# Performance work log

Hardware: AMD Instinct MI355X
Metric: run time of the kernel (lower is better)

## Reference

```python
import jax, jax.numpy as jnp
import numpy as np

N_NODES = 20000
N_EDGES = 200000
F = 132            # features_dim
DEGREES = (1, 2, 3)
REPEATS = jnp.array([3, 5, 7])   # 2l+1
EV_DIM = 15
H_INV, D_INV = 4, 33   # num_heads, inv_head_dim
H_EV, D_EV = 3, 44     # len(degrees), ev_head_dim
NRB = 32


def so3_invariants(x, y):
    # per-degree inner product over the (2l+1) components -> [E, len(degrees)]
    p = x * y
    return jnp.stack([p[:, 0:3].sum(-1), p[:, 3:8].sum(-1), p[:, 8:15].sum(-1)], axis=-1)


def filter_net(rbf, evi, Wr1, br1, Wr2, br2, We1, be1, We2, be2):
    # mlp_rbf: Linear(nrb,F)->SiLU->Linear(F,F); mlp_ev: Linear(3,F//4)->SiLU->Linear(F//4,F)
    r = jax.nn.silu(rbf @ Wr1 + br1) @ Wr2 + br2
    e = jax.nn.silu(evi @ We1 + be1) @ We2 + be2
    return r + e


def setup_inputs() -> dict:
    key = jax.random.key(0)
    ks = jax.random.split(key, 32)
    s = 0.05
    inp = {
        'inv_features': jax.random.normal(ks[0], (N_NODES, F), jnp.float32),
        'ev_features': jax.random.normal(ks[1], (N_NODES, EV_DIM), jnp.float32),
        'rbf': jax.random.uniform(ks[2], (N_EDGES, NRB), jnp.float32),
        'senders': jax.random.randint(ks[3], (N_EDGES,), 0, N_NODES, jnp.int32),
        'receivers': jax.random.randint(ks[4], (N_EDGES,), 0, N_NODES, jnp.int32),
        'sh_vectors': jax.random.normal(ks[5], (N_EDGES, EV_DIM), jnp.float32),
        'cutoffs': jax.random.uniform(ks[6], (N_EDGES, 1), jnp.float32),
        # attention weights
        'W_q_inv': jax.random.normal(ks[7], (H_INV, D_INV, D_INV), jnp.float32) * s,
        'W_k_inv': jax.random.normal(ks[8], (H_INV, D_INV, D_INV), jnp.float32) * s,
        'W_v_inv': jax.random.normal(ks[9], (H_INV, D_INV, D_INV), jnp.float32) * s,
        'W_q_ev': jax.random.normal(ks[10], (H_EV, D_EV, D_EV), jnp.float32) * s,
        'W_k_ev': jax.random.normal(ks[11], (H_EV, D_EV, D_EV), jnp.float32) * s,
    }
    # two FilterNets (inv and ev), stored as [in,out] matrices
    for tag, base in (('fi', 12), ('fe', 20)):
        inp[f'{tag}_rbf_W1'] = jax.random.normal(ks[base + 0], (NRB, F), jnp.float32) * s
        inp[f'{tag}_rbf_b1'] = jnp.zeros((F,), jnp.float32)
        inp[f'{tag}_rbf_W2'] = jax.random.normal(ks[base + 1], (F, F), jnp.float32) * s
        inp[f'{tag}_rbf_b2'] = jnp.zeros((F,), jnp.float32)
        inp[f'{tag}_ev_W1'] = jax.random.normal(ks[base + 2], (len(DEGREES), F // 4), jnp.float32) * s
        inp[f'{tag}_ev_b1'] = jnp.zeros((F // 4,), jnp.float32)
        inp[f'{tag}_ev_W2'] = jax.random.normal(ks[base + 3], (F // 4, F), jnp.float32) * s
        inp[f'{tag}_ev_b2'] = jnp.zeros((F,), jnp.float32)
    # interaction block linear: (F+len(degrees)) -> (F+len(degrees))
    inp['W_int'] = jax.random.normal(ks[28], (F + len(DEGREES), F + len(DEGREES)), jnp.float32) * s
    inp['b_int'] = jnp.zeros((F + len(DEGREES),), jnp.float32)
    return inp


def _forward(inv_features, ev_features, rbf, sh_vectors, cutoffs,
             W_q_inv, W_k_inv, W_v_inv, W_q_ev, W_k_ev,
             fi, fe, W_int, b_int, senders, receivers):
    E = rbf.shape[0]
    N = inv_features.shape[0]
    # ---- EuclideanAttentionBlock ----
    ev_diff = ev_features[senders] - ev_features[receivers]          # [E, 15]
    evi = so3_invariants(ev_diff, ev_diff)                            # [E, 3]
    fw_inv = filter_net(rbf, evi, *fi).reshape(E, H_INV, D_INV)
    fw_ev = filter_net(rbf, evi, *fe).reshape(E, H_EV, D_EV)
    x_inv = inv_features.reshape(N, H_INV, D_INV)
    x_ev = inv_features.reshape(N, H_EV, D_EV)
    q_inv = jnp.einsum('Hij,NHi->NHj', W_q_inv, x_inv)[receivers]
    k_inv = jnp.einsum('Hij,NHi->NHj', W_k_inv, x_inv)[senders]
    v_inv = jnp.einsum('Hij,NHi->NHj', W_v_inv, x_inv)[senders]
    q_ev = jnp.einsum('Hij,NHi->NHj', W_q_ev, x_ev)[receivers]
    k_ev = jnp.einsum('Hij,NHi->NHj', W_k_ev, x_ev)[senders]
    alpha_inv = (q_inv * k_inv * fw_inv).sum(-1, keepdims=True) / np.sqrt(D_INV)  # [E,H,1]
    scaled_inv = cutoffs[:, None] * alpha_inv * v_inv                 # [E,H,D]
    d_inv = jax.ops.segment_sum(scaled_inv, receivers, num_segments=N).reshape(N, F)
    alpha_ev = (q_ev * k_ev * fw_ev).sum(-1) / np.sqrt(D_EV)          # [E,3]
    alpha_ev = jnp.repeat(alpha_ev, REPEATS, axis=-1, total_repeat_length=EV_DIM)
    d_ev = jax.ops.segment_sum(cutoffs * alpha_ev * sh_vectors, receivers, num_segments=N)
    att_inv = inv_features + d_inv
    att_ev = ev_features + d_ev
    # ---- InteractionBlock ----
    evi2 = so3_invariants(att_ev, att_ev)                             # [N,3]
    t = jnp.concatenate([att_inv, evi2], axis=-1) @ W_int + b_int
    d_inv2, b_ev = t[:, :F], t[:, F:]
    d_ev2 = jnp.repeat(b_ev, REPEATS, axis=-1, total_repeat_length=EV_DIM) * att_ev
    return att_inv + d_inv2, att_ev + d_ev2


def reference(inv_features, ev_features, rbf, senders, receivers, sh_vectors, cutoffs,
              W_q_inv, W_k_inv, W_v_inv, W_q_ev, W_k_ev,
              fi_rbf_W1, fi_rbf_b1, fi_rbf_W2, fi_rbf_b2, fi_ev_W1, fi_ev_b1, fi_ev_W2, fi_ev_b2,
              fe_rbf_W1, fe_rbf_b1, fe_rbf_W2, fe_rbf_b2, fe_ev_W1, fe_ev_b1, fe_ev_W2, fe_ev_b2,
              W_int, b_int):
    fi = (fi_rbf_W1, fi_rbf_b1, fi_rbf_W2, fi_rbf_b2, fi_ev_W1, fi_ev_b1, fi_ev_W2, fi_ev_b2)
    fe = (fe_rbf_W1, fe_rbf_b1, fe_rbf_W2, fe_rbf_b2, fe_ev_W1, fe_ev_b1, fe_ev_W2, fe_ev_b2)
    return _forward(inv_features, ev_features, rbf, sh_vectors, cutoffs,
                    W_q_inv, W_k_inv, W_v_inv, W_q_ev, W_k_ev,
                    fi, fe, W_int, b_int, senders, receivers)
```

## Files before the change

### kernel.cpp

```cpp
#include <hip/hip_runtime.h>


#define NN 20000
#define NE 200000
#define FD 132
#define RB 32
#define EVD 15
#define TE 64
#define KPAD 200
#define KG 192
#define NP 144
#define PNT 28
#define FNT 28

typedef __attribute__((ext_vector_type(8))) short bf16x8;
typedef __attribute__((ext_vector_type(4))) float f32x4;

__device__ __forceinline__ float silu_f(float x) {
    return x / (1.0f + __expf(-x));
}
__device__ __forceinline__ unsigned short f2bf(float x) {
    union { float f; unsigned u; } v; v.f = x;
    unsigned r = v.u + 0x7FFF + ((v.u >> 16) & 1);
    return (unsigned short)(r >> 16);
}

__global__ __launch_bounds__(256) void k_prep(
    const float* __restrict__ Wq, const float* __restrict__ Wk, const float* __restrict__ Wv,
    const float* __restrict__ fiW1, const float* __restrict__ fiW2, const float* __restrict__ fiWe2,
    const float* __restrict__ feW1, const float* __restrict__ feW2, const float* __restrict__ feWe2,
    unsigned short* __restrict__ W1Tfi, unsigned short* __restrict__ W1Tfe,
    unsigned short* __restrict__ W2Tfi, unsigned short* __restrict__ W2Tfe,
    float* __restrict__ WqP, float* __restrict__ WkP, float* __restrict__ WvP)
{
    const int gid = blockIdx.x * 256 + threadIdx.x;
    const int gs  = gridDim.x * 256;
    for (int idx = gid; idx < NP * RB; idx += gs) {
        int n = idx / RB, k = idx - n * RB;
        W1Tfi[idx] = f2bf((n < FD) ? fiW1[k * FD + n] : 0.0f);
        W1Tfe[idx] = f2bf((n < FD) ? feW1[k * FD + n] : 0.0f);
    }
    for (int idx = gid; idx < NP * KG; idx += gs) {
        int n = idx / KG, k = idx - n * KG;
        float vi = 0.0f, ve = 0.0f;
        if (n < FD) {
            if (k < FD)       { vi = fiW2[k * FD + n];          ve = feW2[k * FD + n]; }
            else if (k < 165) { vi = fiWe2[(k - FD) * FD + n];  ve = feWe2[(k - FD) * FD + n]; }
        }
        W2Tfi[idx] = f2bf(vi);
        W2Tfe[idx] = f2bf(ve);
    }
    for (int idx = gid; idx < 4 * 33 * 36; idx += gs) {
        int H = idx / (33 * 36), rem = idx - H * (33 * 36);
        int i = rem / 36, jp = rem - i * 36;
        float q = 0.f, k = 0.f, v = 0.f;
        if (jp < 33) {
            q = Wq[H * 1089 + i * 33 + jp];
            k = Wk[H * 1089 + i * 33 + jp];
            v = Wv[H * 1089 + i * 33 + jp];
        }
        WqP[idx] = q; WkP[idx] = k; WvP[idx] = v;
    }
}

__global__ __launch_bounds__(256) void k_hist(const int* __restrict__ rcv,
                                              int* __restrict__ cnt)
{
    int e = blockIdx.x * 256 + threadIdx.x;
    if (e < NE) atomicAdd(&cnt[rcv[e]], 1);
}

__global__ __launch_bounds__(1024) void k_scan(int* __restrict__ cnt_cursor,
                                               int* __restrict__ roff)
{
    __shared__ int sums[1024];
    const int t = threadIdx.x;
    const int base = t * 20;
    int loc[20];
    int s = 0;
    #pragma unroll
    for (int i = 0; i < 20; ++i) {
        int idx = base + i;
        int v = (idx < NN) ? cnt_cursor[idx] : 0;
        loc[i] = s; s += v;
    }
    sums[t] = s;
    __syncthreads();
    for (int off = 1; off < 1024; off <<= 1) {
        int v2 = (t >= off) ? sums[t - off] : 0;
        __syncthreads();
        sums[t] += v2;
        __syncthreads();
    }
    int ex = (t > 0) ? sums[t - 1] : 0;
    #pragma unroll
    for (int i = 0; i < 20; ++i) {
        int idx = base + i;
        if (idx < NN) { roff[idx] = ex + loc[i]; cnt_cursor[idx] = ex + loc[i]; }
    }
    if (t == 1023) roff[NN] = sums[1023];
}

__global__ __launch_bounds__(256) void k_fill(const int* __restrict__ rcv,
                                              int* __restrict__ cursor,
                                              int* __restrict__ eid)
{
    int e = blockIdx.x * 256 + threadIdx.x;
    if (e < NE) {
        int p = atomicAdd(&cursor[rcv[e]], 1);
        eid[p] = e;
    }
}

__global__ __launch_bounds__(256) void k_eprep(
    const float* __restrict__ ev, const int* __restrict__ snd,
    const int* __restrict__ rcv, const float* __restrict__ cut,
    const int* __restrict__ eid,
    float* __restrict__ evi_s, float* __restrict__ cut_s,
    int* __restrict__ ss, int* __restrict__ rs)
{
    int p = blockIdx.x * 256 + threadIdx.x;
    if (p >= NE) return;
    int e = eid[p];
    int s = snd[e], r = rcv[e];
    ss[p] = s; rs[p] = r; cut_s[p] = cut[e];
    const float* ps = &ev[s * EVD];
    const float* pr = &ev[r * EVD];
    float s0 = 0.f, s1 = 0.f, s2 = 0.f;
    #pragma unroll
    for (int m = 0; m < 3; ++m)  { float d = ps[m] - pr[m]; s0 = fmaf(d, d, s0); }
    #pragma unroll
    for (int m = 3; m < 8; ++m)  { float d = ps[m] - pr[m]; s1 = fmaf(d, d, s1); }
    #pragma unroll
    for (int m = 8; m < 15; ++m) { float d = ps[m] - pr[m]; s2 = fmaf(d, d, s2); }
    evi_s[p * 3 + 0] = s0; evi_s[p * 3 + 1] = s1; evi_s[p * 3 + 2] = s2;
}

__device__ __forceinline__ void proj_inv_pass(
    const float* __restrict__ wb, const float (*__restrict__ xT)[PNT],
    float* __restrict__ outp, int t, int n0)
{
    const int q = t % 36, g = t / 36;
    if (g >= 7) return;
    const int H = q / 9, jb = (q - H * 9) * 4, nb = g * 4;
    const int fb = H * 33;
    float acc[4][4] = {};
    for (int i = 0; i < 33; ++i) {
        const float4 w = *(const float4*)&wb[(fb + i) * 36 + jb];
        const float4 x = *(const float4*)&xT[fb + i][nb];
        const float xs[4] = {x.x, x.y, x.z, x.w};
        const float ws[4] = {w.x, w.y, w.z, w.w};
        #pragma unroll
        for (int r = 0; r < 4; ++r)
            #pragma unroll
            for (int c = 0; c < 4; ++c)
                acc[r][c] = fmaf(ws[c], xs[r], acc[r][c]);
    }
    #pragma unroll
    for (int c = 0; c < 4; ++c) {
        int jj = jb + c;
        if (jj >= 33) break;
        int j = H * 33 + jj;
        #pragma unroll
        for (int r = 0; r < 4; ++r) {
            int n = n0 + nb + r;
            if (n < NN) outp[n * FD + j] = acc[r][c];
        }
    }
}

__device__ __forceinline__ void proj_ev_pass(
    const float* __restrict__ wb, const float (*__restrict__ xT)[PNT],
    float* __restrict__ outp, int t, int n0)
{
    const int q = t % 33, g = t / 33;
    if (g >= 7) return;
    const int H = q / 11, jb = (q - H * 11) * 4, nb = g * 4;
    const int fb = H * 44;
    float acc[4][4] = {};
    for (int i = 0; i < 44; ++i) {
        const float4 w = *(const float4*)&wb[(fb + i) * 44 + jb];
        const float4 x = *(const float4*)&xT[fb + i][nb];
        const float xs[4] = {x.x, x.y, x.z, x.w};
        const float ws[4] = {w.x, w.y, w.z, w.w};
        #pragma unroll
        for (int r = 0; r < 4; ++r)
            #pragma unroll
            for (int c = 0; c < 4; ++c)
                acc[r][c] = fmaf(ws[c], xs[r], acc[r][c]);
    }
    #pragma unroll
    for (int c = 0; c < 4; ++c) {
        int j = fb + jb + c;
        #pragma unroll
        for (int r = 0; r < 4; ++r) {
            int n = n0 + nb + r;
            if (n < NN) outp[n * FD + j] = acc[r][c];
        }
    }
}

__global__ __launch_bounds__(256) void k_proj(
    const float* __restrict__ xin,
    const float* __restrict__ WqP, const float* __restrict__ WkP, const float* __restrict__ WvP,
    const float* __restrict__ Wqe, const float* __restrict__ Wke,
    float* __restrict__ qinv, float* __restrict__ kinv, float* __restrict__ vinv,
    float* __restrict__ qev, float* __restrict__ kev)
{
    __shared__ __align__(16) float xT[FD][PNT];
    __shared__ __align__(16) float wb[5808];
    const int t = threadIdx.x;
    const int n0 = blockIdx.x * PNT;

    for (int idx = t; idx < PNT * FD; idx += 256) {
        int nl = idx / FD, j = idx - nl * FD;
        int n = n0 + nl;
        xT[j][nl] = (n < NN) ? xin[n * FD + j] : 0.0f;
    }
    for (int idx = t; idx < 4752; idx += 256) wb[idx] = WqP[idx];
    __syncthreads();
    proj_inv_pass(wb, xT, qinv, t, n0);
    __syncthreads();
    for (int idx = t; idx < 4752; idx += 256) wb[idx] = WkP[idx];
    __syncthreads();
    proj_inv_pass(wb, xT, kinv, t, n0);
    __syncthreads();
    for (int idx = t; idx < 4752; idx += 256) wb[idx] = WvP[idx];
    __syncthreads();
    proj_inv_pass(wb, xT, vinv, t, n0);
    __syncthreads();
    for (int idx = t; idx < 5808; idx += 256) wb[idx] = Wqe[idx];
    __syncthreads();
    proj_ev_pass(wb, xT, qev, t, n0);
    __syncthreads();
    for (int idx = t; idx < 5808; idx += 256) wb[idx] = Wke[idx];
    __syncthreads();
    proj_ev_pass(wb, xT, kev, t, n0);
}

template<int PATH>
__global__ __launch_bounds__(256, 4) void k_edge(
    const float* __restrict__ rbf, const float* __restrict__ evi_s,
    const int* __restrict__ eid, const int* __restrict__ ss,
    const int* __restrict__ rs, const float* __restrict__ cut_s,
    const unsigned short* __restrict__ W1T,
    const float* __restrict__ b1,
    const unsigned short* __restrict__ W2T,
    const float* __restrict__ b2,
    const float* __restrict__ We1, const float* __restrict__ be1,
    const float* __restrict__ be2,
    const float* __restrict__ qt, const float* __restrict__ kt,
    float* __restrict__ aout)
{
    constexpr int   DH = (PATH == 0) ? 33 : 44;
    constexpr float SC = (PATH == 0) ? 0.17407765595569785f : 0.15075567228888181f;

    __shared__ __align__(16) char lds_buf[TE * FD * 4];
    __shared__ float evl[TE * 3];
    __shared__ int   sl[TE];
    __shared__ int   rl[TE];
    __shared__ float cl[TE];

    typedef unsigned short (*HTp)[KPAD];
    HTp HT    = (HTp)lds_buf;
    float* FW = (float*)lds_buf;

    const int t    = threadIdx.x;
    const int wv   = t >> 6;
    const int ln   = t & 63;
    const int lrow = ln & 15;
    const int kseg = ln >> 4;
    const int p0   = blockIdx.x * TE;

    const int  prow = p0 + 16 * wv + lrow;
    const int  eorg = eid[prow];
    const float4 ra = *(const float4*)&rbf[(size_t)eorg * RB + kseg * 8];
    const float4 rb = *(const float4*)&rbf[(size_t)eorg * RB + kseg * 8 + 4];

    if (t < TE) {
        sl[t] = ss[p0 + t];
        rl[t] = rs[p0 + t];
        cl[t] = cut_s[p0 + t];
    }
    for (int idx = t; idx < TE * 3; idx += 256) evl[idx] = evi_s[p0 * 3 + idx];
    __syncthreads();

    {
        bf16x8 afrag;
        afrag[0] = (short)f2bf(ra.x); afrag[1] = (short)f2bf(ra.y);
        afrag[2] = (short)f2bf(ra.z); afrag[3] = (short)f2bf(ra.w);
        afrag[4] = (short)f2bf(rb.x); afrag[5] = (short)f2bf(rb.y);
        afrag[6] = (short)f2bf(rb.z); afrag[7] = (short)f2bf(rb.w);
        #pragma unroll
        for (int nt = 0; nt < 9; ++nt) {
            const int ncol = nt * 16 + lrow;
            bf16x8 bfrag = *(const bf16x8*)&W1T[ncol * RB + kseg * 8];
            f32x4 acc = {0.f, 0.f, 0.f, 0.f};
            acc = __builtin_amdgcn_mfma_f32_16x16x32_bf16(afrag, bfrag, acc, 0, 0, 0);
            if (ncol < FD) {
                const float bias = b1[ncol];
                #pragma unroll
                for (int r = 0; r < 4; ++r)
                    HT[16 * wv + kseg * 4 + r][ncol] = f2bf(silu_f(acc[r] + bias));
            }
        }
    }
    for (int idx = t; idx < TE * 33; idx += 256) {
        int e = idx / 33, ii = idx - e * 33;
        float a = be1[ii];
        a = fmaf(evl[e * 3 + 0], We1[ii], a);
        a = fmaf(evl[e * 3 + 1], We1[33 + ii], a);
        a = fmaf(evl[e * 3 + 2], We1[66 + ii], a);
        HT[e][FD + ii] = f2bf(silu_f(a));
    }
    for (int idx = t; idx < TE * (KPAD - 165); idx += 256) {
        int e = idx / (KPAD - 165), kk = idx - e * (KPAD - 165);
        HT[e][165 + kk] = 0;
    }
    __syncthreads();

    f32x4 acc[9];
    #pragma unroll
    for (int nt = 0; nt < 9; ++nt) acc[nt] = (f32x4){0.f, 0.f, 0.f, 0.f};
    {
        const unsigned short* hrow = &HT[16 * wv + lrow][0];
        #pragma unroll
        for (int kt = 0; kt < 6; ++kt) {
            bf16x8 afrag = *(const bf16x8*)&hrow[kt * 32 + kseg * 8];
            #pragma unroll
            for (int nt = 0; nt < 9; ++nt) {
                bf16x8 bfrag = *(const bf16x8*)&W2T[(nt * 16 + lrow) * KG + kt * 32 + kseg * 8];
                acc[nt] = __builtin_amdgcn_mfma_f32_16x16x32_bf16(afrag, bfrag, acc[nt], 0, 0, 0);
            }
        }
    }
    __syncthreads();

    #pragma unroll
    for (int nt = 0; nt < 9; ++nt) {
        const int ncol = nt * 16 + lrow;
        if (ncol < FD) {
            const float bias = b2[ncol] + be2[ncol];
            #pragma unroll
            for (int r = 0; r < 4; ++r)
                FW[(16 * wv + kseg * 4 + r) * FD + ncol] = acc[nt][r] + bias;
        }
    }
    __syncthreads();

    {
        const int eq = t >> 2;
        const int m  = t & 3;
        const int jb = m * 33;
        const float* qp = qt + (size_t)rl[eq] * FD + jb;
        const float* kp = kt + (size_t)sl[eq] * FD + jb;
        const float* fp = &FW[eq * FD + jb];
        const int hlo   = jb / DH;
        const int split = (PATH == 0) ? 33 : (DH * (hlo + 1) - jb);
        float pa = 0.f, pb = 0.f;
        #pragma unroll
        for (int jj = 0; jj < 33; ++jj) {
            float f = fp[jj] * qp[jj] * kp[jj];
            if (jj < split) pa += f; else pb += f;
        }
        float nxt = __shfl_down(pa, 1);
        if (PATH == 0) {
            aout[(size_t)(p0 + eq) * 4 + m] = pa * cl[eq] * SC;
        } else {
            if (m < 3) {
                float a = ((m == 0) ? pa : pb) + nxt;
                aout[(size_t)(p0 + eq) * 4 + m] = a * cl[eq] * SC;
            }
        }
    }
}

__global__ __launch_bounds__(256) void k_final(
    const float* __restrict__ xin, const float* __restrict__ evf,
    const float* __restrict__ vt, const float* __restrict__ sh,
    const float* __restrict__ alphaI, const float* __restrict__ alphaE,
    const int* __restrict__ roff, const int* __restrict__ eid,
    const int* __restrict__ ss,
    const float* __restrict__ Wint, const float* __restrict__ bint,
    float* __restrict__ out)
{
    __shared__ __align__(16) float catT[136][FNT];
    __shared__ float aev[FNT][16];
    __shared__ float tacc[FNT][4];
    const int t = threadIdx.x;
    const int n0 = blockIdx.x * FNT;
    const int wv = t >> 6, ln = t & 63;

    const int h0 = ln / 33;
    const int h1 = (64 + ln) / 33;
    const int hm = (ln < 3) ? 0 : ((ln < 8) ? 1 : 2);
    for (int nl = wv; nl < FNT; nl += 4) {
        const int n = n0 + nl;
        float a0 = 0.f, a1 = 0.f, a2 = 0.f, dv = 0.f;
        if (n < NN) {
            const int pend = roff[n + 1];
            int p = roff[n];
            for (; p + 2 <= pend; p += 2) {
                const int sA = ss[p], sB = ss[p + 1];
                const int eA = eid[p], eB = eid[p + 1];
                const float* vA = vt + (size_t)sA * FD;
                const float* vB = vt + (size_t)sB * FD;
                const float aA0 = alphaI[(size_t)p * 4 + h0];
                const float aB0 = alphaI[(size_t)(p + 1) * 4 + h0];
                const float aA1 = alphaI[(size_t)p * 4 + h1];
                const float aB1 = alphaI[(size_t)(p + 1) * 4 + h1];
                a0 = fmaf(aA0, vA[ln], a0);      a0 = fmaf(aB0, vB[ln], a0);
                a1 = fmaf(aA1, vA[64 + ln], a1); a1 = fmaf(aB1, vB[64 + ln], a1);
                if (ln < 4) {
                    a2 = fmaf(alphaI[(size_t)p * 4 + 3], vA[128 + ln], a2);
                    a2 = fmaf(alphaI[(size_t)(p + 1) * 4 + 3], vB[128 + ln], a2);
                }
                if (ln < 15) {
                    dv = fmaf(alphaE[(size_t)p * 4 + hm], sh[(size_t)eA * EVD + ln], dv);
                    dv = fmaf(alphaE[(size_t)(p + 1) * 4 + hm], sh[(size_t)eB * EVD + ln], dv);
                }
            }
            for (; p < pend; ++p) {
                const int sA = ss[p];
                const int eA = eid[p];
                const float* vA = vt + (size_t)sA * FD;
                a0 = fmaf(alphaI[(size_t)p * 4 + h0], vA[ln], a0);
                a1 = fmaf(alphaI[(size_t)p * 4 + h1], vA[64 + ln], a1);
                if (ln < 4)  a2 = fmaf(alphaI[(size_t)p * 4 + 3], vA[128 + ln], a2);
                if (ln < 15) dv = fmaf(alphaE[(size_t)p * 4 + hm], sh[(size_t)eA * EVD + ln], dv);
            }
            catT[ln][nl]      = xin[n * FD + ln]      + a0;
            catT[64 + ln][nl] = xin[n * FD + 64 + ln] + a1;
            if (ln < 4)  catT[128 + ln][nl] = xin[n * FD + 128 + ln] + a2;
            if (ln < 15) aev[nl][ln] = evf[n * EVD + ln] + dv;
        } else {
            catT[ln][nl] = 0.f; catT[64 + ln][nl] = 0.f;
            if (ln < 4)  catT[128 + ln][nl] = 0.f;
            if (ln < 15) aev[nl][ln] = 0.f;
        }
    }
    if (t < FNT) catT[135][t] = 0.0f;
    __syncthreads();
    if (t < FNT * 3) {
        int nl = t / 3, k = t - nl * 3;
        int lo = (k == 0) ? 0 : ((k == 1) ? 3 : 8);
        int hi = (k == 0) ? 3 : ((k == 1) ? 8 : 15);
        float s = 0.f;
        for (int m = lo; m < hi; ++m) { float v = aev[nl][m]; s = fmaf(v, v, s); }
        catT[FD + k][nl] = s;
    }
    __syncthreads();

    const int q = t % 34, g = t / 34;
    const int jb = q * 4, nb = g * 4;
    const bool act = (g < 7);
    float acc[4][4] = {};
    if (act) {
        #pragma unroll 5
        for (int c = 0; c < 135; ++c) {
            const float* wr = Wint + c * 135 + jb;
            const float w0 = wr[0];
            const float w1 = wr[1];
            const float w2 = wr[2];
            const float w3 = (jb + 3 < 135) ? wr[3] : 0.f;
            const float4 x = *(const float4*)&catT[c][nb];
            const float xs[4] = {x.x, x.y, x.z, x.w};
            #pragma unroll
            for (int r = 0; r < 4; ++r) {
                acc[r][0] = fmaf(w0, xs[r], acc[r][0]);
                acc[r][1] = fmaf(w1, xs[r], acc[r][1]);
                acc[r][2] = fmaf(w2, xs[r], acc[r][2]);
                acc[r][3] = fmaf(w3, xs[r], acc[r][3]);
            }
        }
        #pragma unroll
        for (int c = 0; c < 4; ++c) {
            int j = jb + c;
            if (j >= 135) break;
            float bj = bint[j];
            #pragma unroll
            for (int r = 0; r < 4; ++r) {
                int n = n0 + nb + r;
                if (n >= NN) continue;
                float a = acc[r][c] + bj;
                if (j < FD) out[n * FD + j] = catT[j][nb + r] + a;
                else        tacc[nb + r][j - FD] = a;
            }
        }
    }
    __syncthreads();
    for (int idx = t; idx < FNT * EVD; idx += 256) {
        int nl = idx / EVD, m = idx - nl * EVD;
        int n = n0 + nl;
        if (n >= NN) continue;
        int hd = (m < 3) ? 0 : ((m < 8) ? 1 : 2);
        out[NN * FD + n * EVD + m] = aev[nl][m] * (1.0f + tacc[nl][hd]);
    }
}

extern "C" void kernel_launch(void* const* d_in, const int* in_sizes, int n_in,
                              void* d_out, int out_size, void* d_ws, size_t ws_size,
                              hipStream_t stream)
{
    (void)in_sizes; (void)n_in; (void)out_size; (void)ws_size;
    const float* xin  = (const float*)d_in[0];
    const float* evf  = (const float*)d_in[1];
    const float* rbf  = (const float*)d_in[2];
    const int*   snd  = (const int*)d_in[3];
    const int*   rcv  = (const int*)d_in[4];
    const float* sh   = (const float*)d_in[5];
    const float* cut  = (const float*)d_in[6];
    const float* Wint = (const float*)d_in[28];
    const float* bint = (const float*)d_in[29];

    float* ws     = (float*)d_ws;
    float* qinv   = ws;
    float* kinv   = qinv   + NN * FD;
    float* vinv   = kinv   + NN * FD;
    float* qev    = vinv   + NN * FD;
    float* kev    = qev    + NN * FD;
    float* alphaI = kev    + NN * FD;
    float* alphaE = alphaI + NE * 4;
    float* evi_s  = alphaE + NE * 4;
    float* cut_s  = evi_s  + NE * 3;
    int*   iwork  = (int*)(cut_s + NE);
    int*   roff   = iwork;
    int*   cnt_cursor = roff + (NN + 1);
    int*   eid    = cnt_cursor + NN;
    int*   ss     = eid + NE;
    int*   rs     = ss + NE;
    float* wtail  = (float*)(iwork + 640004);

    unsigned short* W2Tfi = (unsigned short*)wtail;
    unsigned short* W2Tfe = W2Tfi + NP * KG;
    unsigned short* W1Tfi = W2Tfe + NP * KG;
    unsigned short* W1Tfe = W1Tfi + NP * RB;
    float* WqP = (float*)(W1Tfe + NP * RB);
    float* WkP = WqP + 4 * 33 * 36;
    float* WvP = WkP + 4 * 33 * 36;

    hipMemsetAsync(cnt_cursor, 0, (size_t)NN * sizeof(int), stream);
    k_hist<<<(NE + 255) / 256, 256, 0, stream>>>(rcv, cnt_cursor);
    k_scan<<<1, 1024, 0, stream>>>(cnt_cursor, roff);
    k_fill<<<(NE + 255) / 256, 256, 0, stream>>>(rcv, cnt_cursor, eid);
    k_eprep<<<(NE + 255) / 256, 256, 0, stream>>>(evf, snd, rcv, cut, eid,
                                                  evi_s, cut_s, ss, rs);

    k_prep<<<64, 256, 0, stream>>>(
        (const float*)d_in[7], (const float*)d_in[8], (const float*)d_in[9],
        (const float*)d_in[12], (const float*)d_in[14], (const float*)d_in[18],
        (const float*)d_in[20], (const float*)d_in[22], (const float*)d_in[26],
        W1Tfi, W1Tfe, W2Tfi, W2Tfe, WqP, WkP, WvP);

    k_proj<<<(NN + PNT - 1) / PNT, 256, 0, stream>>>(
        xin, WqP, WkP, WvP,
        (const float*)d_in[10], (const float*)d_in[11],
        qinv, kinv, vinv, qev, kev);

    const int nt = NE / TE;
    k_edge<0><<<nt, 256, 0, stream>>>(rbf, evi_s, eid, ss, rs, cut_s,
        W1Tfi, (const float*)d_in[13], W2Tfi, (const float*)d_in[15],
        (const float*)d_in[16], (const float*)d_in[17], (const float*)d_in[19],
        qinv, kinv, alphaI);
    k_edge<1><<<nt, 256, 0, stream>>>(rbf, evi_s, eid, ss, rs, cut_s,
        W1Tfe, (const float*)d_in[21], W2Tfe, (const float*)d_in[23],
        (const float*)d_in[24], (const float*)d_in[25], (const float*)d_in[27],
        qev, kev, alphaE);

    k_final<<<(NN + FNT - 1) / FNT, 256, 0, stream>>>(
        xin, evf, vinv, sh, alphaI, alphaE, roff, eid, ss,
        Wint, bint, (float*)d_out);
}
```

Measured before the change: 657.8 us.

## Fuse both edge filter paths into one single-wave kernel per 16 edges

Merges the two per-path edge kernels into one kernel where each 64-thread block handles 16 edges and runs the inv path and then the ev path. The rbf fragment, edge indices, cutoffs and invariants are loaded once and shared by both paths instead of being gathered twice, and one kernel launch goes away. Blocks shrink from four waves to one, which cuts LDS per block and makes barriers cheaper but raises the block count and reduces reuse of W2T loads across waves within a block.

```diff
diff --git a/kernel.cpp b/kernel.cpp
--- a/kernel.cpp
+++ b/kernel.cpp
@@ -6,7 +6,7 @@
 #define FD 132
 #define RB 32
 #define EVD 15
-#define TE 64
+#define WE 16
 #define KPAD 200
 #define KG 192
 #define NP 144
@@ -239,73 +239,36 @@
 }
 
 template<int PATH>
-__global__ __launch_bounds__(256, 4) void k_edge(
-    const float* __restrict__ rbf, const float* __restrict__ evi_s,
-    const int* __restrict__ eid, const int* __restrict__ ss,
-    const int* __restrict__ rs, const float* __restrict__ cut_s,
-    const unsigned short* __restrict__ W1T,
-    const float* __restrict__ b1,
-    const unsigned short* __restrict__ W2T,
-    const float* __restrict__ b2,
+__device__ __forceinline__ void edge_path(
+    bf16x8 afrag,
+    unsigned short (*__restrict__ HT)[KPAD], float* __restrict__ FW,
+    const float* __restrict__ evl, const int* __restrict__ sl,
+    const int* __restrict__ rl, const float* __restrict__ cl,
+    const unsigned short* __restrict__ W1T, const float* __restrict__ b1,
+    const unsigned short* __restrict__ W2T, const float* __restrict__ b2,
     const float* __restrict__ We1, const float* __restrict__ be1,
     const float* __restrict__ be2,
     const float* __restrict__ qt, const float* __restrict__ kt,
-    float* __restrict__ aout)
+    float* __restrict__ aout,
+    int ln, int lrow, int kseg, int p0)
 {
     constexpr int   DH = (PATH == 0) ? 33 : 44;
     constexpr float SC = (PATH == 0) ? 0.17407765595569785f : 0.15075567228888181f;
 
-    __shared__ __align__(16) char lds_buf[TE * FD * 4];
-    __shared__ float evl[TE * 3];
-    __shared__ int   sl[TE];
-    __shared__ int   rl[TE];
-    __shared__ float cl[TE];
-
-    typedef unsigned short (*HTp)[KPAD];
-    HTp HT    = (HTp)lds_buf;
-    float* FW = (float*)lds_buf;
-
-    const int t    = threadIdx.x;
-    const int wv   = t >> 6;
-    const int ln   = t & 63;
-    const int lrow = ln & 15;
-    const int kseg = ln >> 4;
-    const int p0   = blockIdx.x * TE;
-
-    const int  prow = p0 + 16 * wv + lrow;
-    const int  eorg = eid[prow];
-    const float4 ra = *(const float4*)&rbf[(size_t)eorg * RB + kseg * 8];
-    const float4 rb = *(const float4*)&rbf[(size_t)eorg * RB + kseg * 8 + 4];
-
-    if (t < TE) {
-        sl[t] = ss[p0 + t];
-        rl[t] = rs[p0 + t];
-        cl[t] = cut_s[p0 + t];
-    }
-    for (int idx = t; idx < TE * 3; idx += 256) evl[idx] = evi_s[p0 * 3 + idx];
-    __syncthreads();
-
-    {
-        bf16x8 afrag;
-        afrag[0] = (short)f2bf(ra.x); afrag[1] = (short)f2bf(ra.y);
-        afrag[2] = (short)f2bf(ra.z); afrag[3] = (short)f2bf(ra.w);
-        afrag[4] = (short)f2bf(rb.x); afrag[5] = (short)f2bf(rb.y);
-        afrag[6] = (short)f2bf(rb.z); afrag[7] = (short)f2bf(rb.w);
-        #pragma unroll
-        for (int nt = 0; nt < 9; ++nt) {
-            const int ncol = nt * 16 + lrow;
-            bf16x8 bfrag = *(const bf16x8*)&W1T[ncol * RB + kseg * 8];
-            f32x4 acc = {0.f, 0.f, 0.f, 0.f};
-            acc = __builtin_amdgcn_mfma_f32_16x16x32_bf16(afrag, bfrag, acc, 0, 0, 0);
-            if (ncol < FD) {
-                const float bias = b1[ncol];
-                #pragma unroll
-                for (int r = 0; r < 4; ++r)
-                    HT[16 * wv + kseg * 4 + r][ncol] = f2bf(silu_f(acc[r] + bias));
-            }
-        }
-    }
-    for (int idx = t; idx < TE * 33; idx += 256) {
+    #pragma unroll
+    for (int nt = 0; nt < 9; ++nt) {
+        const int ncol = nt * 16 + lrow;
+        bf16x8 bfrag = *(const bf16x8*)&W1T[ncol * RB + kseg * 8];
+        f32x4 acc = {0.f, 0.f, 0.f, 0.f};
+        acc = __builtin_amdgcn_mfma_f32_16x16x32_bf16(afrag, bfrag, acc, 0, 0, 0);
+        if (ncol < FD) {
+            const float bias = b1[ncol];
+            #pragma unroll
+            for (int r = 0; r < 4; ++r)
+                HT[kseg * 4 + r][ncol] = f2bf(silu_f(acc[r] + bias));
+        }
+    }
+    for (int idx = ln; idx < WE * 33; idx += 64) {
         int e = idx / 33, ii = idx - e * 33;
         float a = be1[ii];
         a = fmaf(evl[e * 3 + 0], We1[ii], a);
@@ -313,7 +276,7 @@
         a = fmaf(evl[e * 3 + 2], We1[66 + ii], a);
         HT[e][FD + ii] = f2bf(silu_f(a));
     }
-    for (int idx = t; idx < TE * (KPAD - 165); idx += 256) {
+    for (int idx = ln; idx < WE * (KPAD - 165); idx += 64) {
         int e = idx / (KPAD - 165), kk = idx - e * (KPAD - 165);
         HT[e][165 + kk] = 0;
     }
@@ -323,14 +286,14 @@
     #pragma unroll
     for (int nt = 0; nt < 9; ++nt) acc[nt] = (f32x4){0.f, 0.f, 0.f, 0.f};
     {
-        const unsigned short* hrow = &HT[16 * wv + lrow][0];
+        const unsigned short* hrow = &HT[lrow][0];
         #pragma unroll
         for (int kt = 0; kt < 6; ++kt) {
-            bf16x8 afrag = *(const bf16x8*)&hrow[kt * 32 + kseg * 8];
+            bf16x8 af = *(const bf16x8*)&hrow[kt * 32 + kseg * 8];
             #pragma unroll
             for (int nt = 0; nt < 9; ++nt) {
                 bf16x8 bfrag = *(const bf16x8*)&W2T[(nt * 16 + lrow) * KG + kt * 32 + kseg * 8];
-                acc[nt] = __builtin_amdgcn_mfma_f32_16x16x32_bf16(afrag, bfrag, acc[nt], 0, 0, 0);
+                acc[nt] = __builtin_amdgcn_mfma_f32_16x16x32_bf16(af, bfrag, acc[nt], 0, 0, 0);
             }
         }
     }
@@ -343,14 +306,14 @@
             const float bias = b2[ncol] + be2[ncol];
             #pragma unroll
             for (int r = 0; r < 4; ++r)
-                FW[(16 * wv + kseg * 4 + r) * FD + ncol] = acc[nt][r] + bias;
+                FW[(kseg * 4 + r) * FD + ncol] = acc[nt][r] + bias;
         }
     }
     __syncthreads();
 
     {
-        const int eq = t >> 2;
-        const int m  = t & 3;
+        const int eq = ln >> 2;
+        const int m  = ln & 3;
         const int jb = m * 33;
         const float* qp = qt + (size_t)rl[eq] * FD + jb;
         const float* kp = kt + (size_t)sl[eq] * FD + jb;
@@ -373,6 +336,64 @@
             }
         }
     }
+}
+
+__global__ __launch_bounds__(64, 4) void k_edge2(
+    const float* __restrict__ rbf, const float* __restrict__ evi_s,
+    const int* __restrict__ eid, const int* __restrict__ ss,
+    const int* __restrict__ rs, const float* __restrict__ cut_s,
+    const unsigned short* __restrict__ W1Ti, const float* __restrict__ b1i,
+    const unsigned short* __restrict__ W2Ti, const float* __restrict__ b2i,
+    const float* __restrict__ We1i, const float* __restrict__ be1i,
+    const float* __restrict__ be2i,
+    const float* __restrict__ qti, const float* __restrict__ kti,
+    float* __restrict__ aoutI,
+    const unsigned short* __restrict__ W1Te, const float* __restrict__ b1e,
+    const unsigned short* __restrict__ W2Te, const float* __restrict__ b2e,
+    const float* __restrict__ We1e, const float* __restrict__ be1e,
+    const float* __restrict__ be2e,
+    const float* __restrict__ qte, const float* __restrict__ kte,
+    float* __restrict__ aoutE)
+{
+    __shared__ __align__(16) char lds_buf[WE * FD * 4];
+    __shared__ float evl[WE * 3];
+    __shared__ int   sl[WE];
+    __shared__ int   rl[WE];
+    __shared__ float cl[WE];
+
+    typedef unsigned short (*HTp)[KPAD];
+    HTp HT    = (HTp)lds_buf;
+    float* FW = (float*)lds_buf;
+
+    const int ln   = threadIdx.x;
+    const int lrow = ln & 15;
+    const int kseg = ln >> 4;
+    const int p0   = blockIdx.x * WE;
+
+    const int eorg = eid[p0 + lrow];
+    const float4 ra = *(const float4*)&rbf[(size_t)eorg * RB + kseg * 8];
+    const float4 rb = *(const float4*)&rbf[(size_t)eorg * RB + kseg * 8 + 4];
+    bf16x8 afrag;
+    afrag[0] = (short)f2bf(ra.x); afrag[1] = (short)f2bf(ra.y);
+    afrag[2] = (short)f2bf(ra.z); afrag[3] = (short)f2bf(ra.w);
+    afrag[4] = (short)f2bf(rb.x); afrag[5] = (short)f2bf(rb.y);
+    afrag[6] = (short)f2bf(rb.z); afrag[7] = (short)f2bf(rb.w);
+
+    if (ln < WE) {
+        sl[ln] = ss[p0 + ln];
+        rl[ln] = rs[p0 + ln];
+        cl[ln] = cut_s[p0 + ln];
+    }
+    if (ln < WE * 3) evl[ln] = evi_s[p0 * 3 + ln];
+    __syncthreads();
+
+    edge_path<0>(afrag, HT, FW, evl, sl, rl, cl,
+                 W1Ti, b1i, W2Ti, b2i, We1i, be1i, be2i, qti, kti, aoutI,
+                 ln, lrow, kseg, p0);
+    __syncthreads();
+    edge_path<1>(afrag, HT, FW, evl, sl, rl, cl,
+                 W1Te, b1e, W2Te, b2e, We1e, be1e, be2e, qte, kte, aoutE,
+                 ln, lrow, kseg, p0);
 }
 
 __global__ __launch_bounds__(256) void k_final(
@@ -557,12 +578,10 @@
         (const float*)d_in[10], (const float*)d_in[11],
         qinv, kinv, vinv, qev, kev);
 
-    const int nt = NE / TE;
-    k_edge<0><<<nt, 256, 0, stream>>>(rbf, evi_s, eid, ss, rs, cut_s,
+    k_edge2<<<NE / WE, 64, 0, stream>>>(rbf, evi_s, eid, ss, rs, cut_s,
         W1Tfi, (const float*)d_in[13], W2Tfi, (const float*)d_in[15],
         (const float*)d_in[16], (const float*)d_in[17], (const float*)d_in[19],
-        qinv, kinv, alphaI);
-    k_edge<1><<<nt, 256, 0, stream>>>(rbf, evi_s, eid, ss, rs, cut_s,
+        qinv, kinv, alphaI,
         W1Tfe, (const float*)d_in[21], W2Tfe, (const float*)d_in[23],
         (const float*)d_in[24], (const float*)d_in[25], (const float*)d_in[27],
         qev, kev, alphaE);
```

After: 646.1 us. No clear change (-1.8%).
